# Kernel optimization log

Measured on AMD Instinct MI355X. Metric: run time of the kernel, lower is better.

The kernel has to match this reference:

```python
import jax, jax.numpy as jnp
import numpy as np

D = 256
N = 131072


def setup_inputs() -> dict:
    key = jax.random.key(0)
    kx, ku = jax.random.split(key)
    X = jax.random.normal(kx, (N, D), dtype=jnp.float32)
    U = jax.random.normal(ku, (D, D), dtype=jnp.float32) * 0.5
    # reset_parameters: normalize each row of U
    U = U / jnp.linalg.norm(U, axis=1, keepdims=True)
    return {"X": X, "U": U}


def reference(X, U):
    # sequential_mult iterates rows from d-1 down to 0, so scan over flipped U.
    def step(Xc, v):
        # v: [d];  X <- X - 2 * (X v) v^T / (v.v)
        coef = (Xc @ v) * (2.0 / jnp.dot(v, v))  # [N]
        Xc = Xc - coef[:, None] * v[None, :]
        return Xc, None

    Xout, _ = jax.lax.scan(step, X, U[::-1])
    return Xout
```

## Files before the change

### kernel.cpp

```cpp
#include <hip/hip_runtime.h>
#include <hip/hip_bf16.h>

typedef __attribute__((ext_vector_type(8))) short short8;
typedef __attribute__((ext_vector_type(4))) float f32x4;

#define DDIM 256
#define NROWS 131072
#define RG 256
#define GBLK (RG * 2)
#define RPG (NROWS / RG)
#define CHUNK 128
#define NSTEP 32

static __device__ __forceinline__ unsigned short f2bf(float f){
  unsigned b = __builtin_bit_cast(unsigned, f);
  b += 0x7FFFu + ((b >> 16) & 1u);
  return (unsigned short)(b >> 16);
}

static __device__ __forceinline__ float wave_sum_bcast(float x){
  int v = __builtin_bit_cast(int, x);
#define DPP_ADD(ctrl)                                                          \
  v = __builtin_bit_cast(int,                                                  \
        __builtin_bit_cast(float, v) +                                         \
        __builtin_bit_cast(float,                                              \
          __builtin_amdgcn_update_dpp(0, v, (ctrl), 0xF, 0xF, true)))
  DPP_ADD(0x111);
  DPP_ADD(0x112);
  DPP_ADD(0x114);
  DPP_ADD(0x118);
  DPP_ADD(0x142);
  DPP_ADD(0x143);
#undef DPP_ADD
  return __builtin_bit_cast(float, __builtin_amdgcn_readlane(v, 63));
}

__global__ __launch_bounds__(256) void compute_q(const float* __restrict__ U,
                                                 unsigned short* __restrict__ Qt){
  const int lane = threadIdx.x & 63;
  const int wv   = threadIdx.x >> 6;
  const int pair = blockIdx.x * 4 + wv;
  const int j0 = pair * 2, j1 = j0 + 1;

  float u0[4], u1[4], r0[4], r1[4], r2[4], r3[4];
#pragma unroll
  for (int e = 0; e < 4; ++e){
    const int i = e * 64 + lane;
    u0[e] = (i == j0) ? 1.f : 0.f;
    u1[e] = (i == j1) ? 1.f : 0.f;
    r0[e] = U[0 * 256 + i];
    r1[e] = U[1 * 256 + i];
    r2[e] = U[2 * 256 + i];
    r3[e] = U[3 * 256 + i];
  }

#define QSTEP(R, KN)                                                           \
  do {                                                                         \
    const float p0_ = (u0[0]*R[0] + u0[1]*R[1]) + (u0[2]*R[2] + u0[3]*R[3]);   \
    const float p1_ = (u1[0]*R[0] + u1[1]*R[1]) + (u1[2]*R[2] + u1[3]*R[3]);   \
    const float pv_ = (R[0]*R[0] + R[1]*R[1]) + (R[2]*R[2] + R[3]*R[3]);       \
    const float d0_ = wave_sum_bcast(p0_);                                     \
    const float d1_ = wave_sum_bcast(p1_);                                     \
    const float dv_ = wave_sum_bcast(pv_);                                     \
    const float inv_ = 2.0f * __builtin_amdgcn_rcpf(dv_);                      \
    const float c0_ = d0_ * inv_, c1_ = d1_ * inv_;                            \
    _Pragma("unroll")                                                          \
    for (int e = 0; e < 4; ++e){                                               \
      u0[e] = fmaf(-c0_, R[e], u0[e]);                                         \
      u1[e] = fmaf(-c1_, R[e], u1[e]);                                         \
      R[e] = U[(size_t)(KN) * 256 + e * 64 + lane];                            \
    }                                                                          \
  } while (0)

  for (int k = 0; k < 256; k += 4){
    const int k4 = (k+4) & 255, k5 = (k+5) & 255, k6 = (k+6) & 255, k7 = (k+7) & 255;
    QSTEP(r0, k4);
    QSTEP(r1, k5);
    QSTEP(r2, k6);
    QSTEP(r3, k7);
  }
#undef QSTEP

#pragma unroll
  for (int e = 0; e < 4; ++e){
    const int i = e * 64 + lane;
    Qt[(size_t)j0 * 256 + i] = f2bf(u0[e]);
    Qt[(size_t)j1 * 256 + i] = f2bf(u1[e]);
  }
}

__global__ __launch_bounds__(512, 4) void gemm_xq(const float* __restrict__ X,
                                                  const unsigned short* __restrict__ Qt,
                                                  float* __restrict__ Y){
  __shared__ char qb[65536];

  const int tid  = threadIdx.x;
  const int lane = tid & 63;
  const int wv   = tid >> 6;
  const int lg   = lane >> 4;
  const int lm   = lane & 15;
  const int half = blockIdx.x & 1;
  const size_t rg = blockIdx.x >> 1;
  const size_t rowbase = rg * RPG;

  f32x4 sv[8];
#pragma unroll
  for (int it = 0; it < 8; ++it){
    const int c = tid + it * 512;
    sv[it] = *reinterpret_cast<const f32x4*>(
        reinterpret_cast<const char*>(Qt) +
        ((size_t)(half * 128) << 9) + ((size_t)c << 4));
  }

  const float* xl = X + (rowbase + wv * 16 + lm) * DDIM + lg * 8;

  f32x4 f[4][2];
#define LDX(slot, s)                                                           \
  do {                                                                         \
    const float* p_ = xl + (size_t)((s) >> 3) * (CHUNK * DDIM) + ((s) & 7) * 32;\
    f[slot][0] = *reinterpret_cast<const f32x4*>(p_);                          \
    f[slot][1] = *reinterpret_cast<const f32x4*>(p_ + 4);                      \
  } while (0)

  LDX(0, 0); LDX(1, 1); LDX(2, 2); LDX(3, 3);

#pragma unroll
  for (int it = 0; it < 8; ++it){
    const int c   = tid + it * 512;
    const int n   = c >> 5;
    const int off = (c & 31) << 4;
    *reinterpret_cast<f32x4*>(qb + (n << 9) + (off ^ ((n & 15) << 5))) = sv[it];
  }
  __syncthreads();

  f32x4 acc[8];
#pragma unroll
  for (int nt = 0; nt < 8; ++nt) acc[nt] = (f32x4){0.f, 0.f, 0.f, 0.f};

#pragma unroll
  for (int s = 0; s < NSTEP; ++s){
    {
      const f32x4 lo = f[s & 3][0], hi = f[s & 3][1];
      short8 a;
      a[0] = (short)f2bf(lo[0]); a[1] = (short)f2bf(lo[1]);
      a[2] = (short)f2bf(lo[2]); a[3] = (short)f2bf(lo[3]);
      a[4] = (short)f2bf(hi[0]); a[5] = (short)f2bf(hi[1]);
      a[6] = (short)f2bf(hi[2]); a[7] = (short)f2bf(hi[3]);
      const int kb = (s & 7) * 64 + (lg << 4);
#pragma unroll
      for (int nt = 0; nt < 8; ++nt){
        const int nl = nt * 16 + lm;
        const short8 b = *reinterpret_cast<const short8*>(
            qb + (nl << 9) + (kb ^ ((nl & 15) << 5)));
        acc[nt] = __builtin_amdgcn_mfma_f32_16x16x32_bf16(a, b, acc[nt], 0, 0, 0);
      }
    }
    if (s + 4 < NSTEP) LDX(s & 3, s + 4);
    if ((s & 7) == 7){
      const int c = s >> 3;
      const size_t orow = rowbase + (size_t)c * CHUNK + wv * 16 + lg * 4;
#pragma unroll
      for (int nt = 0; nt < 8; ++nt){
#pragma unroll
        for (int r = 0; r < 4; ++r){
          Y[(orow + r) * DDIM + half * 128 + nt * 16 + lm] = acc[nt][r];
        }
        acc[nt] = (f32x4){0.f, 0.f, 0.f, 0.f};
      }
    }
  }
#undef LDX
}

extern "C" void kernel_launch(void* const* d_in, const int* in_sizes, int n_in,
                              void* d_out, int out_size, void* d_ws, size_t ws_size,
                              hipStream_t stream) {
  const float* X = (const float*)d_in[0];
  const float* U = (const float*)d_in[1];
  float* Y = (float*)d_out;
  unsigned short* Qt = (unsigned short*)d_ws;

  compute_q<<<32, 256, 0, stream>>>(U, Qt);
  gemm_xq<<<GBLK, 512, 0, stream>>>(X, Qt, Y);
}
```

Baseline: 120.0 us.

## Stage X tiles into an LDS ring via async global-to-LDS loads

Replaces register-prefetched X loads with global_load_lds transfers into a 5-slot swizzled LDS ring, issued three tiles ahead. Hand-computed vmcnt waits plus barriers order each tile before it is consumed. Q is also loaded straight into LDS, and outputs use nontemporal stores. The aim is deeper memory latency hiding and fewer VGPRs spent on prefetch, at the cost of about 144KB of LDS per block (lower occupancy) and a barrier on every tile.

Result: slower. 123.0 us (+2.6%).

```diff
diff --git a/kernel.cpp b/kernel.cpp
--- a/kernel.cpp
+++ b/kernel.cpp
@@ -9,8 +9,11 @@
 #define RG 256
 #define GBLK (RG * 2)
 #define RPG (NROWS / RG)
-#define CHUNK 128
-#define NSTEP 32
+#define TROWS 128
+#define NTILE 32
+#define RING 5
+#define AHEAD 3
+#define XTILE 16384
 
 static __device__ __forceinline__ unsigned short f2bf(float f){
   unsigned b = __builtin_bit_cast(unsigned, f);
@@ -25,12 +28,8 @@
         __builtin_bit_cast(float, v) +                                         \
         __builtin_bit_cast(float,                                              \
           __builtin_amdgcn_update_dpp(0, v, (ctrl), 0xF, 0xF, true)))
-  DPP_ADD(0x111);
-  DPP_ADD(0x112);
-  DPP_ADD(0x114);
-  DPP_ADD(0x118);
-  DPP_ADD(0x142);
-  DPP_ADD(0x143);
+  DPP_ADD(0x111); DPP_ADD(0x112); DPP_ADD(0x114); DPP_ADD(0x118);
+  DPP_ADD(0x142); DPP_ADD(0x143);
 #undef DPP_ADD
   return __builtin_bit_cast(float, __builtin_amdgcn_readlane(v, 63));
 }
@@ -74,10 +73,7 @@
 
   for (int k = 0; k < 256; k += 4){
     const int k4 = (k+4) & 255, k5 = (k+5) & 255, k6 = (k+6) & 255, k7 = (k+7) & 255;
-    QSTEP(r0, k4);
-    QSTEP(r1, k5);
-    QSTEP(r2, k6);
-    QSTEP(r3, k7);
+    QSTEP(r0, k4); QSTEP(r1, k5); QSTEP(r2, k6); QSTEP(r3, k7);
   }
 #undef QSTEP
 
@@ -89,10 +85,25 @@
   }
 }
 
-__global__ __launch_bounds__(512, 4) void gemm_xq(const float* __restrict__ X,
-                                                  const unsigned short* __restrict__ Qt,
-                                                  float* __restrict__ Y){
-  __shared__ char qb[65536];
+static __device__ __forceinline__ void gl16(const void* g, void* l){
+  __builtin_amdgcn_global_load_lds(
+      (const __attribute__((address_space(1))) unsigned int*)g,
+      (__attribute__((address_space(3))) unsigned int*)l, 16, 0, 0);
+}
+
+__host__ __device__ constexpr int wcnt(int t){
+  const int rem = (NTILE - 1) - t;
+  const int inflight = rem < AHEAD ? rem : AHEAD;
+  int w = 2 * inflight;
+  if (t >= 8 && (t & 7) <= (AHEAD - 1)) w += 32;
+  return w;
+}
+
+__global__ __launch_bounds__(512) void gemm_xq(const float* __restrict__ X,
+                                               const unsigned short* __restrict__ Qt,
+                                               float* __restrict__ Y){
+  __shared__ __attribute__((aligned(16))) char qb[65536];
+  __shared__ __attribute__((aligned(16))) char ring[RING * XTILE];
 
   const int tid  = threadIdx.x;
   const int lane = tid & 63;
@@ -100,76 +111,95 @@
   const int lg   = lane >> 4;
   const int lm   = lane & 15;
   const int half = blockIdx.x & 1;
-  const size_t rg = blockIdx.x >> 1;
-  const size_t rowbase = rg * RPG;
-
-  f32x4 sv[8];
-#pragma unroll
-  for (int it = 0; it < 8; ++it){
-    const int c = tid + it * 512;
-    sv[it] = *reinterpret_cast<const f32x4*>(
-        reinterpret_cast<const char*>(Qt) +
-        ((size_t)(half * 128) << 9) + ((size_t)c << 4));
-  }
-
-  const float* xl = X + (rowbase + wv * 16 + lm) * DDIM + lg * 8;
-
-  f32x4 f[4][2];
-#define LDX(slot, s)                                                           \
-  do {                                                                         \
-    const float* p_ = xl + (size_t)((s) >> 3) * (CHUNK * DDIM) + ((s) & 7) * 32;\
-    f[slot][0] = *reinterpret_cast<const f32x4*>(p_);                          \
-    f[slot][1] = *reinterpret_cast<const f32x4*>(p_ + 4);                      \
-  } while (0)
-
-  LDX(0, 0); LDX(1, 1); LDX(2, 2); LDX(3, 3);
-
-#pragma unroll
-  for (int it = 0; it < 8; ++it){
-    const int c   = tid + it * 512;
-    const int n   = c >> 5;
-    const int off = (c & 31) << 4;
-    *reinterpret_cast<f32x4*>(qb + (n << 9) + (off ^ ((n & 15) << 5))) = sv[it];
-  }
-  __syncthreads();
+  const size_t rowbase = (size_t)(blockIdx.x >> 1) * RPG;
+
+  {
+    const char* qsrc = (const char*)Qt + ((size_t)half * 128) * 512;
+#pragma unroll
+    for (int it = 0; it < 8; ++it){
+      const int c  = tid + it * 512;
+      const int nl = c >> 5;
+      const int sl = (c & 31) ^ ((nl & 15) << 1);
+      gl16(qsrc + (size_t)nl * 512 + sl * 16, qb + (it * 512 + wv * 64) * 16);
+    }
+  }
+
+#define STAGE(u) do{                                                           \
+    char* sb_ = ring + ((u) % RING) * XTILE;                                   \
+    const char* gb_ = (const char*)X +                                         \
+        (rowbase + (size_t)((u) >> 3) * TROWS) * 1024 + ((u) & 7) * 128;       \
+    { const int c_ = tid;       const int r_ = c_ >> 3;                        \
+      const int sl_ = (c_ & 7) ^ (r_ & 7);                                     \
+      gl16(gb_ + (size_t)r_ * 1024 + sl_ * 16, sb_ + (wv * 64) * 16); }        \
+    { const int c_ = tid + 512; const int r_ = c_ >> 3;                        \
+      const int sl_ = (c_ & 7) ^ (r_ & 7);                                     \
+      gl16(gb_ + (size_t)r_ * 1024 + sl_ * 16, sb_ + (512 + wv * 64) * 16); }  \
+  }while(0)
+
+  STAGE(0); STAGE(1); STAGE(2);
 
   f32x4 acc[8];
 #pragma unroll
-  for (int nt = 0; nt < 8; ++nt) acc[nt] = (f32x4){0.f, 0.f, 0.f, 0.f};
-
-#pragma unroll
-  for (int s = 0; s < NSTEP; ++s){
-    {
-      const f32x4 lo = f[s & 3][0], hi = f[s & 3][1];
-      short8 a;
-      a[0] = (short)f2bf(lo[0]); a[1] = (short)f2bf(lo[1]);
-      a[2] = (short)f2bf(lo[2]); a[3] = (short)f2bf(lo[3]);
-      a[4] = (short)f2bf(hi[0]); a[5] = (short)f2bf(hi[1]);
-      a[6] = (short)f2bf(hi[2]); a[7] = (short)f2bf(hi[3]);
-      const int kb = (s & 7) * 64 + (lg << 4);
-#pragma unroll
-      for (int nt = 0; nt < 8; ++nt){
-        const int nl = nt * 16 + lm;
-        const short8 b = *reinterpret_cast<const short8*>(
-            qb + (nl << 9) + (kb ^ ((nl & 15) << 5)));
-        acc[nt] = __builtin_amdgcn_mfma_f32_16x16x32_bf16(a, b, acc[nt], 0, 0, 0);
-      }
-    }
-    if (s + 4 < NSTEP) LDX(s & 3, s + 4);
-    if ((s & 7) == 7){
-      const int c = s >> 3;
-      const size_t orow = rowbase + (size_t)c * CHUNK + wv * 16 + lg * 4;
-#pragma unroll
-      for (int nt = 0; nt < 8; ++nt){
-#pragma unroll
-        for (int r = 0; r < 4; ++r){
-          Y[(orow + r) * DDIM + half * 128 + nt * 16 + lm] = acc[nt][r];
-        }
-        acc[nt] = (f32x4){0.f, 0.f, 0.f, 0.f};
-      }
-    }
-  }
-#undef LDX
+  for (int i = 0; i < 8; ++i) acc[i] = (f32x4){0.f, 0.f, 0.f, 0.f};
+
+  const int xrow = wv * 16 + lm;
+  const int xsw  = (xrow & 7) << 4;
+
+#define CONSUME(u) do{                                                         \
+    const char* sb_ = ring + ((u) % RING) * XTILE;                             \
+    const f32x4 xa_ = *(const f32x4*)(sb_ + xrow * 128 + ((lg * 32)      ^ xsw));\
+    const f32x4 xb_ = *(const f32x4*)(sb_ + xrow * 128 + ((lg * 32 + 16) ^ xsw));\
+    short8 a_;                                                                 \
+    a_[0] = (short)f2bf(xa_[0]); a_[1] = (short)f2bf(xa_[1]);                  \
+    a_[2] = (short)f2bf(xa_[2]); a_[3] = (short)f2bf(xa_[3]);                  \
+    a_[4] = (short)f2bf(xb_[0]); a_[5] = (short)f2bf(xb_[1]);                  \
+    a_[6] = (short)f2bf(xb_[2]); a_[7] = (short)f2bf(xb_[3]);                  \
+    const int kb_ = ((u) & 7) * 64 + (lg << 4);                                \
+    _Pragma("unroll")                                                          \
+    for (int nt_ = 0; nt_ < 8; ++nt_){                                         \
+      const int nl_ = nt_ * 16 + lm;                                           \
+      const short8 b_ = *(const short8*)(qb + (nl_ << 9) +                     \
+                                         (kb_ ^ ((nl_ & 15) << 5)));           \
+      acc[nt_] = __builtin_amdgcn_mfma_f32_16x16x32_bf16(a_, b_, acc[nt_],     \
+                                                         0, 0, 0);             \
+    }                                                                          \
+  }while(0)
+
+#define STORECHUNK(c) do{                                                      \
+    const size_t orow_ = rowbase + (size_t)(c) * TROWS + wv * 16 + lg * 4;     \
+    _Pragma("unroll")                                                          \
+    for (int nt_ = 0; nt_ < 8; ++nt_){                                         \
+      _Pragma("unroll")                                                        \
+      for (int r_ = 0; r_ < 4; ++r_){                                          \
+        __builtin_nontemporal_store(acc[nt_][r_],                              \
+            &Y[(orow_ + r_) * DDIM + half * 128 + nt_ * 16 + lm]);             \
+      }                                                                        \
+      acc[nt_] = (f32x4){0.f, 0.f, 0.f, 0.f};                                  \
+    }                                                                          \
+  }while(0)
+
+#define PHASE(t) do{                                                           \
+    if ((t) + AHEAD < NTILE) STAGE((t) + AHEAD);                               \
+    asm volatile("s_waitcnt vmcnt(%0)" :: "n"(wcnt(t)) : "memory");            \
+    __builtin_amdgcn_s_barrier();                                              \
+    __builtin_amdgcn_sched_barrier(0);                                         \
+    CONSUME(t);                                                                \
+    if (((t) & 7) == 7) STORECHUNK((t) >> 3);                                  \
+  }while(0)
+
+  PHASE(0);  PHASE(1);  PHASE(2);  PHASE(3);
+  PHASE(4);  PHASE(5);  PHASE(6);  PHASE(7);
+  PHASE(8);  PHASE(9);  PHASE(10); PHASE(11);
+  PHASE(12); PHASE(13); PHASE(14); PHASE(15);
+  PHASE(16); PHASE(17); PHASE(18); PHASE(19);
+  PHASE(20); PHASE(21); PHASE(22); PHASE(23);
+  PHASE(24); PHASE(25); PHASE(26); PHASE(27);
+  PHASE(28); PHASE(29); PHASE(30); PHASE(31);
+
+#undef PHASE
+#undef STORECHUNK
+#undef CONSUME
+#undef STAGE
 }
 
 extern "C" void kernel_launch(void* const* d_in, const int* in_sizes, int n_in,
```

## Compute full 256-column output per block to avoid reading X twice

Applied to the files above, without the earlier changes.

The GEMM no longer splits output columns into two halves across blocks. Each of 256 blocks of 1024 threads now holds the whole 128KB bf16 Q in LDS and computes all 256 output columns for its 512 rows, so each X row is loaded and converted to bf16 once instead of twice. The X prefetch depth drops from 4 to 3 to keep register pressure in check with 16 accumulators. The cost is one block per CU because of the LDS size, fewer blocks than before, and less latency hiding.

Measured after the change: 194.8 us. +62.4%, slower.

```diff
diff --git a/kernel.cpp b/kernel.cpp
--- a/kernel.cpp
+++ b/kernel.cpp
@@ -6,11 +6,9 @@
 
 #define DDIM 256
 #define NROWS 131072
-#define RG 256
-#define GBLK (RG * 2)
-#define RPG (NROWS / RG)
-#define CHUNK 128
-#define NSTEP 32
+#define GBLK 256
+#define RPB (NROWS / GBLK)
+#define NSTEP 16
 
 static __device__ __forceinline__ unsigned short f2bf(float f){
   unsigned b = __builtin_bit_cast(unsigned, f);
@@ -25,12 +23,8 @@
         __builtin_bit_cast(float, v) +                                         \
         __builtin_bit_cast(float,                                              \
           __builtin_amdgcn_update_dpp(0, v, (ctrl), 0xF, 0xF, true)))
-  DPP_ADD(0x111);
-  DPP_ADD(0x112);
-  DPP_ADD(0x114);
-  DPP_ADD(0x118);
-  DPP_ADD(0x142);
-  DPP_ADD(0x143);
+  DPP_ADD(0x111); DPP_ADD(0x112); DPP_ADD(0x114); DPP_ADD(0x118);
+  DPP_ADD(0x142); DPP_ADD(0x143);
 #undef DPP_ADD
   return __builtin_bit_cast(float, __builtin_amdgcn_readlane(v, 63));
 }
@@ -74,10 +68,7 @@
 
   for (int k = 0; k < 256; k += 4){
     const int k4 = (k+4) & 255, k5 = (k+5) & 255, k6 = (k+6) & 255, k7 = (k+7) & 255;
-    QSTEP(r0, k4);
-    QSTEP(r1, k5);
-    QSTEP(r2, k6);
-    QSTEP(r3, k7);
+    QSTEP(r0, k4); QSTEP(r1, k5); QSTEP(r2, k6); QSTEP(r3, k7);
   }
 #undef QSTEP
 
@@ -89,58 +80,55 @@
   }
 }
 
-__global__ __launch_bounds__(512, 4) void gemm_xq(const float* __restrict__ X,
-                                                  const unsigned short* __restrict__ Qt,
-                                                  float* __restrict__ Y){
-  __shared__ char qb[65536];
+__global__ __launch_bounds__(1024) void gemm_xq(const float* __restrict__ X,
+                                                const unsigned short* __restrict__ Qt,
+                                                float* __restrict__ Y){
+  __shared__ char qb[131072];
 
   const int tid  = threadIdx.x;
   const int lane = tid & 63;
   const int wv   = tid >> 6;
   const int lg   = lane >> 4;
   const int lm   = lane & 15;
-  const int half = blockIdx.x & 1;
-  const size_t rg = blockIdx.x >> 1;
-  const size_t rowbase = rg * RPG;
+  const size_t rowbase = (size_t)blockIdx.x * RPB;
 
   f32x4 sv[8];
 #pragma unroll
   for (int it = 0; it < 8; ++it){
-    const int c = tid + it * 512;
+    const int c = tid + it * 1024;
     sv[it] = *reinterpret_cast<const f32x4*>(
-        reinterpret_cast<const char*>(Qt) +
-        ((size_t)(half * 128) << 9) + ((size_t)c << 4));
+        reinterpret_cast<const char*>(Qt) + ((size_t)c << 4));
   }
 
   const float* xl = X + (rowbase + wv * 16 + lm) * DDIM + lg * 8;
 
-  f32x4 f[4][2];
+  f32x4 f[3][2];
 #define LDX(slot, s)                                                           \
   do {                                                                         \
-    const float* p_ = xl + (size_t)((s) >> 3) * (CHUNK * DDIM) + ((s) & 7) * 32;\
+    const float* p_ = xl + (size_t)((s) >> 3) * (256 * DDIM) + ((s) & 7) * 32; \
     f[slot][0] = *reinterpret_cast<const f32x4*>(p_);                          \
     f[slot][1] = *reinterpret_cast<const f32x4*>(p_ + 4);                      \
   } while (0)
 
-  LDX(0, 0); LDX(1, 1); LDX(2, 2); LDX(3, 3);
+  LDX(0, 0); LDX(1, 1); LDX(2, 2);
 
 #pragma unroll
   for (int it = 0; it < 8; ++it){
-    const int c   = tid + it * 512;
+    const int c   = tid + it * 1024;
     const int n   = c >> 5;
     const int off = (c & 31) << 4;
     *reinterpret_cast<f32x4*>(qb + (n << 9) + (off ^ ((n & 15) << 5))) = sv[it];
   }
   __syncthreads();
 
-  f32x4 acc[8];
+  f32x4 acc[16];
 #pragma unroll
-  for (int nt = 0; nt < 8; ++nt) acc[nt] = (f32x4){0.f, 0.f, 0.f, 0.f};
+  for (int i = 0; i < 16; ++i) acc[i] = (f32x4){0.f, 0.f, 0.f, 0.f};
 
 #pragma unroll
   for (int s = 0; s < NSTEP; ++s){
     {
-      const f32x4 lo = f[s & 3][0], hi = f[s & 3][1];
+      const f32x4 lo = f[s % 3][0], hi = f[s % 3][1];
       short8 a;
       a[0] = (short)f2bf(lo[0]); a[1] = (short)f2bf(lo[1]);
       a[2] = (short)f2bf(lo[2]); a[3] = (short)f2bf(lo[3]);
@@ -148,22 +136,21 @@
       a[6] = (short)f2bf(hi[2]); a[7] = (short)f2bf(hi[3]);
       const int kb = (s & 7) * 64 + (lg << 4);
 #pragma unroll
-      for (int nt = 0; nt < 8; ++nt){
-        const int nl = nt * 16 + lm;
+      for (int nt = 0; nt < 16; ++nt){
+        const int n = nt * 16 + lm;
         const short8 b = *reinterpret_cast<const short8*>(
-            qb + (nl << 9) + (kb ^ ((nl & 15) << 5)));
+            qb + (n << 9) + (kb ^ ((n & 15) << 5)));
         acc[nt] = __builtin_amdgcn_mfma_f32_16x16x32_bf16(a, b, acc[nt], 0, 0, 0);
       }
     }
-    if (s + 4 < NSTEP) LDX(s & 3, s + 4);
+    if (s + 3 < NSTEP) LDX(s % 3, s + 3);
     if ((s & 7) == 7){
-      const int c = s >> 3;
-      const size_t orow = rowbase + (size_t)c * CHUNK + wv * 16 + lg * 4;
+      const size_t orow = rowbase + (size_t)(s >> 3) * 256 + wv * 16 + lg * 4;
 #pragma unroll
-      for (int nt = 0; nt < 8; ++nt){
+      for (int nt = 0; nt < 16; ++nt){
 #pragma unroll
         for (int r = 0; r < 4; ++r){
-          Y[(orow + r) * DDIM + half * 128 + nt * 16 + lm] = acc[nt][r];
+          Y[(orow + r) * DDIM + nt * 16 + lm] = acc[nt][r];
         }
         acc[nt] = (f32x4){0.f, 0.f, 0.f, 0.f};
       }
@@ -181,5 +168,5 @@
   unsigned short* Qt = (unsigned short*)d_ws;
 
   compute_q<<<32, 256, 0, stream>>>(U, Qt);
-  gemm_xq<<<GBLK, 512, 0, stream>>>(X, Qt, Y);
+  gemm_xq<<<GBLK, 1024, 0, stream>>>(X, Qt, Y);
 }
```
